# Kernel tuning notes

Hardware: AMD Instinct MI355X
Metric: run time of the kernel (lower is better)

The kernel has to match this reference:

```python
import jax, jax.numpy as jnp
import numpy as np

# Module constants (from init_kwargs / MoELayer branch for n_experts=8)
D_MODEL = 512
D_FF = 2048
N_HEADS = 8
N_EXPERTS = 8
TOP_K = 2
CAPACITY_FACTOR = 1.6  # n_experts > 6 branch
BATCH = 4096
SEQ = 16  # 4x4 board
LN_EPS = 1e-5


def setup_inputs() -> dict:
    key = jax.random.key(0)
    ks = jax.random.split(key, 24)
    s = 0.02
    d, f, e = D_MODEL, D_FF, N_EXPERTS
    inp = {
        'x': jax.random.normal(ks[0], (BATCH, SEQ, d), dtype=jnp.float32),
        'ln1_g': jnp.ones((d,), jnp.float32), 'ln1_b': jnp.zeros((d,), jnp.float32),
        'ln2_g': jnp.ones((d,), jnp.float32), 'ln2_b': jnp.zeros((d,), jnp.float32),
        # Linear weights stored [in, out] (equivalent to torch W.T)
        'wq': jax.random.normal(ks[1], (d, d)) * s, 'bq': jnp.zeros((d,)),
        'wk': jax.random.normal(ks[2], (d, d)) * s, 'bk': jnp.zeros((d,)),
        'wv': jax.random.normal(ks[3], (d, d)) * s, 'bv': jnp.zeros((d,)),
        'wo': jax.random.normal(ks[4], (d, d)) * s, 'bo': jnp.zeros((d,)),
        'router_w': jax.random.normal(ks[5], (d, e)) * s, 'router_b': jnp.zeros((e,)),
        'w1': jax.random.normal(ks[6], (e, d, f)) * s, 'b1': jnp.zeros((e, f)),
        'w2': jax.random.normal(ks[7], (e, f, d)) * s, 'b2': jnp.zeros((e, d)),
    }
    return inp


def _layernorm(x, g, b):
    mu = x.mean(-1, keepdims=True)
    var = ((x - mu) ** 2).mean(-1, keepdims=True)
    return (x - mu) * jax.lax.rsqrt(var + LN_EPS) * g + b


def _moe(xf, router_w, router_b, w1, b1, w2, b2):
    # xf: [T, D]
    T = xf.shape[0]
    probs = jax.nn.softmax(xf @ router_w + router_b, axis=-1)  # [T, E]
    _, topk_idx = jax.lax.top_k(probs, TOP_K)                  # [T, K]
    capacity = int(np.ceil(T * CAPACITY_FACTOR / N_EXPERTS))
    out = jnp.zeros_like(xf)
    tok = jnp.arange(T)
    for i in range(N_EXPERTS):
        mask = (topk_idx == i).any(-1)                 # token routed to expert i
        pos = jnp.where(mask, tok, T)                  # sentinel T for unrouted
        sel = jnp.sort(pos)[:capacity]                 # first `capacity` routed tokens, in token order
        xi = xf[jnp.minimum(sel, T - 1)]               # gather (padded rows unused)
        hi = jax.nn.gelu(xi @ w1[i] + b1[i], approximate=False)
        yi = hi @ w2[i] + b2[i]
        # scatter; OOB sentinel indices are dropped. Later experts overwrite
        # earlier ones for tokens routed to multiple experts (matches torch).
        out = out.at[sel].set(yi, mode='drop')
    return out


def reference(x, ln1_g, ln1_b, ln2_g, ln2_b, wq, bq, wk, bk, wv, bv, wo, bo,
              router_w, router_b, w1, b1, w2, b2):
    B, S, D = x.shape
    dk = D // N_HEADS
    # --- attention sublayer ---
    h = _layernorm(x, ln1_g, ln1_b)
    q = (h @ wq + bq).reshape(B, S, N_HEADS, dk)
    k = (h @ wk + bk).reshape(B, S, N_HEADS, dk)
    v = (h @ wv + bv).reshape(B, S, N_HEADS, dk)
    scores = jnp.einsum('bqhd,bkhd->bhqk', q, k) / np.sqrt(dk).astype(np.float32)
    attn = jax.nn.softmax(scores, axis=-1)
    ctx = jnp.einsum('bhqk,bkhd->bqhd', attn, v).reshape(B, S, D)
    x = x + ctx @ wo + bo
    # --- MoE sublayer ---
    h2 = _layernorm(x, ln2_g, ln2_b)
    moe_out = _moe(h2.reshape(-1, D), router_w, router_b, w1, b1, w2, b2)
    return x + moe_out.reshape(B, S, D)
```

## Files before the change

kernel.cpp:

```cpp
#include <hip/hip_runtime.h>
#include <hip/hip_bf16.h>
#include <math.h>

typedef unsigned short u16;
typedef unsigned int u32;
typedef _Float16 f16;
typedef __attribute__((ext_vector_type(8))) _Float16 f16x8;
typedef __attribute__((ext_vector_type(8))) short short8;
typedef __attribute__((ext_vector_type(4))) float f32x4;

#define TTOK 65536
#define QTOK 16384
#define CAP 13108
#define CAPP 13184

#define MFMA16(a, b, c) __builtin_amdgcn_mfma_f32_16x16x32_f16(a, b, c, 0, 0, 0)
#define MFMAB(a, b, c) __builtin_amdgcn_mfma_f32_16x16x32_bf16(a, b, c, 0, 0, 0)
#define LO_SCALE 2.44140625e-4f

#define SWZF(r) (((r) & 3) ^ ((((r) >> 2) & 1) << 1))

__device__ __forceinline__ u16 f2bf(float f) {
  union { float f; u32 u; } v; v.f = f;
  u32 r = v.u + 0x7fffu + ((v.u >> 16) & 1u);
  return (u16)(r >> 16);
}
__device__ __forceinline__ u16 f16b(f16 h) {
  union { f16 h; u16 u; } v; v.h = h; return v.u;
}
__device__ __forceinline__ f16 b2h(u16 u) {
  union { u16 s; f16 h; } v; v.s = u; return v.h;
}
__device__ __forceinline__ float gelu_f(float x) {
  float z = fabsf(x) * 0.70710678118654752f;
  float t = __builtin_amdgcn_rcpf(1.0f + 0.3275911f * z);
  float p = t * (0.254829592f + t * (-0.284496736f + t * (1.421413741f
          + t * (-1.453152027f + t * 1.061405429f))));
  float er = 1.0f - p * __expf(-z * z);
  er = (x < 0.0f) ? -er : er;
  return 0.5f * x * (1.0f + er);
}
__device__ __forceinline__ void gl16(const u16* g, u16* l) {
  __builtin_amdgcn_global_load_lds(
      (const __attribute__((address_space(1))) u32*)(const void*)g,
      (__attribute__((address_space(3))) u32*)(void*)l, 16, 0, 0);
}

__global__ __launch_bounds__(256) void prep1_kernel(
    const float* __restrict__ wq, const float* __restrict__ wk,
    const float* __restrict__ wv, const float* __restrict__ wo,
    const float* __restrict__ rw,
    u16* __restrict__ whi, u16* __restrict__ wlo, float* __restrict__ rwt)
{
  const int z = blockIdx.z;
  int idx = blockIdx.x * 256 + threadIdx.x;
  if (z == 4) {
    if (idx < 4096) {
      int n = idx >> 9, k = idx & 511;
      rwt[idx] = rw[k * 8 + n];
    }
    return;
  }
  const float* src = (z == 0) ? wq : (z == 1) ? wk : (z == 2) ? wv : wo;
  int n = idx >> 9, k = idx & 511;
  float v = src[k * 512 + n];
  f16 h = (f16)v;
  f16 l = (f16)((v - (float)h) * 4096.0f);
  whi[z * 262144 + idx] = f16b(h);
  wlo[z * 262144 + idx] = f16b(l);
}

__global__ __launch_bounds__(256) void prep2_kernel(
    const float* __restrict__ w1, const float* __restrict__ w2,
    u16* __restrict__ w1t, u16* __restrict__ w2t)
{
  __shared__ float tS[64][65];
  const int z = blockIdx.z;
  const float* src; u16* dst; int R, C;
  if (z < 8) { src = w1 + (size_t)z * 1048576; dst = w1t + (size_t)z * 1048576; R = 512; C = 2048; }
  else       { src = w2 + (size_t)(z - 8) * 1048576; dst = w2t + (size_t)(z - 8) * 1048576; R = 2048; C = 512; }
  const int tc = C >> 6;
  const int r0 = (blockIdx.x / tc) * 64, c0 = (blockIdx.x % tc) * 64;
  const int tid = threadIdx.x;
  #pragma unroll
  for (int j = 0; j < 16; ++j) {
    int idx = j * 256 + tid;
    int r = idx >> 6, c = idx & 63;
    tS[r][c] = src[(size_t)(r0 + r) * C + c0 + c];
  }
  __syncthreads();
  #pragma unroll
  for (int j = 0; j < 16; ++j) {
    int idx = j * 256 + tid;
    int c = idx >> 6, r = idx & 63;
    dst[(size_t)(c0 + c) * R + r0 + r] = f2bf(tS[r][c]);
  }
}

__global__ __launch_bounds__(256) void ln1_kernel(
    const float* __restrict__ x, const float* __restrict__ g,
    const float* __restrict__ b, u16* __restrict__ hh, u16* __restrict__ hl)
{
  const int row = blockIdx.x * 4 + (threadIdx.x >> 6);
  const int lane = threadIdx.x & 63;
  const float* xr = x + (size_t)row * 512 + lane * 8;
  float4 a = *(const float4*)xr;
  float4 c = *(const float4*)(xr + 4);
  double s1 = (double)a.x + a.y + a.z + a.w + c.x + c.y + c.z + c.w;
  double s2 = (double)a.x * a.x + (double)a.y * a.y + (double)a.z * a.z + (double)a.w * a.w
            + (double)c.x * c.x + (double)c.y * c.y + (double)c.z * c.z + (double)c.w * c.w;
  #pragma unroll
  for (int off = 32; off; off >>= 1) {
    s1 += __shfl_xor(s1, off, 64);
    s2 += __shfl_xor(s2, off, 64);
  }
  double mu = s1 * (1.0 / 512.0);
  double var = s2 * (1.0 / 512.0) - mu * mu;
  double rs = 1.0 / sqrt(var + 1e-5);
  float4 ga = *(const float4*)(g + lane * 8);
  float4 gb = *(const float4*)(g + lane * 8 + 4);
  float4 ba = *(const float4*)(b + lane * 8);
  float4 bb = *(const float4*)(b + lane * 8 + 4);
  float vv[8] = {a.x, a.y, a.z, a.w, c.x, c.y, c.z, c.w};
  float gg[8] = {ga.x, ga.y, ga.z, ga.w, gb.x, gb.y, gb.z, gb.w};
  float cc[8] = {ba.x, ba.y, ba.z, ba.w, bb.x, bb.y, bb.z, bb.w};
  u16 oh[8], ol[8];
  #pragma unroll
  for (int j = 0; j < 8; ++j) {
    float t = (float)(((double)vv[j] - mu) * rs);
    float n0 = t * gg[j] + cc[j];
    f16 h = (f16)n0;
    oh[j] = f16b(h);
    ol[j] = f16b((f16)((n0 - (float)h) * 4096.0f));
  }
  size_t base = (size_t)row * 512 + lane * 8;
  *(short8*)(hh + base) = *(const short8*)oh;
  *(short8*)(hl + base) = *(const short8*)ol;
}

__global__ __launch_bounds__(512, 2) void qkv_gemm_kernel(
    const u16* __restrict__ hh, const u16* __restrict__ hl,
    const u16* __restrict__ whi, const u16* __restrict__ wlo,
    const float* __restrict__ bq, const float* __restrict__ bk,
    const float* __restrict__ bv, u32* __restrict__ qkvh, int M0)
{
  __shared__ alignas(16) u16 SM[2][16384];
  const int tid = threadIdx.x;
  const int lane = tid & 63, w = tid >> 6;
  const int lid = blockIdx.x + 12 * blockIdx.y;
  const int c8 = lid & 7, kk = lid >> 3;
  const int rt = c8 * 16 + kk / 12;
  const int ct = kk % 12;
  const int col0 = ct * 128;
  const int row0 = rt * 128;
  const int wr = w >> 2, wc = w & 3;
  const int lr = lane & 15, lkq = lane >> 4;
  const int sx = (lkq ^ SWZF(lr)) * 8;
  const int lrow = lane >> 2;
  const int lcs = ((lane & 3) ^ SWZF(lrow)) * 8;

  const u16* gsrc[4];
  int loff[4];
  #pragma unroll
  for (int j = 0; j < 4; ++j) {
    const int q = w * 4 + j;
    loff[j] = q * 512;
    if (q < 8)       gsrc[j] = hh + (size_t)(M0 + row0 + q * 16 + lrow) * 512 + lcs;
    else if (q < 16) gsrc[j] = hl + (size_t)(M0 + row0 + (q - 8) * 16 + lrow) * 512 + lcs;
    else if (q < 24) gsrc[j] = whi + (size_t)(col0 + (q - 16) * 16 + lrow) * 512 + lcs;
    else             gsrc[j] = wlo + (size_t)(col0 + (q - 24) * 16 + lrow) * 512 + lcs;
  }

  f32x4 acch[4][2], accl[4][2];
  #pragma unroll
  for (int m = 0; m < 4; ++m)
    #pragma unroll
    for (int n = 0; n < 2; ++n) {
      f32x4 zz = {0.f, 0.f, 0.f, 0.f};
      acch[m][n] = zz; accl[m][n] = zz;
    }

  #pragma unroll
  for (int j = 0; j < 4; ++j) gl16(gsrc[j], &SM[0][loff[j]]);
  #pragma unroll
  for (int j = 0; j < 4; ++j) gl16(gsrc[j] + 32, &SM[1][loff[j]]);

  for (int kc = 0; kc < 16; ++kc) {
    if (kc == 15) asm volatile("s_waitcnt vmcnt(0)" ::: "memory");
    else          asm volatile("s_waitcnt vmcnt(4)" ::: "memory");
    __builtin_amdgcn_s_barrier();
    __builtin_amdgcn_sched_barrier(0);
    const u16* S = SM[kc & 1];
    f16x8 ah[4], al[4], bh[2], bl[2];
    #pragma unroll
    for (int m = 0; m < 4; ++m) {
      int r = wr * 64 + m * 16 + lr;
      ah[m] = *(const f16x8*)&S[r * 32 + sx];
      al[m] = *(const f16x8*)&S[4096 + r * 32 + sx];
    }
    #pragma unroll
    for (int n = 0; n < 2; ++n) {
      int c = wc * 32 + n * 16 + lr;
      bh[n] = *(const f16x8*)&S[8192 + c * 32 + sx];
      bl[n] = *(const f16x8*)&S[12288 + c * 32 + sx];
    }
    #pragma unroll
    for (int m = 0; m < 4; ++m)
      #pragma unroll
      for (int n = 0; n < 2; ++n) {
        acch[m][n] = MFMA16(ah[m], bh[n], acch[m][n]);
        accl[m][n] = MFMA16(ah[m], bl[n], accl[m][n]);
        accl[m][n] = MFMA16(al[m], bh[n], accl[m][n]);
      }
    __builtin_amdgcn_s_barrier();
    __builtin_amdgcn_sched_barrier(0);
    if (kc + 2 < 16) {
      #pragma unroll
      for (int j = 0; j < 4; ++j) gl16(gsrc[j] + (kc + 2) * 32, &SM[kc & 1][loff[j]]);
    }
  }
  #pragma unroll
  for (int m = 0; m < 4; ++m)
    #pragma unroll
    for (int n = 0; n < 2; ++n) {
      int col = col0 + wc * 32 + n * 16 + lr;
      float bb = (col < 512) ? bq[col] : (col < 1024) ? bk[col - 512] : bv[col - 1024];
      #pragma unroll
      for (int r = 0; r < 4; ++r) {
        int row = row0 + wr * 64 + m * 16 + lkq * 4 + r;
        float val = acch[m][n][r] + accl[m][n][r] * LO_SCALE + bb;
        f16 vh = (f16)val;
        f16 vl = (f16)((val - (float)vh) * 4096.0f);
        qkvh[(size_t)row * 1536 + col] = (u32)f16b(vh) | ((u32)f16b(vl) << 16);
      }
    }
}

__global__ __launch_bounds__(512) void attn_kernel(
    const u32* __restrict__ qkvh, u16* __restrict__ cth, u16* __restrict__ ctl)
{
  __shared__ alignas(16) u32 vS[16384];
  __shared__ float pS[8][16][17];

  const int tid = threadIdx.x;
  const int lane = tid & 63, w = tid >> 6;
  const int lr = lane & 15, lkq = lane >> 4;
  const int row0 = blockIdx.x * 32;

  #pragma unroll
  for (int i = 0; i < 8; ++i) {
    int chunk = w * 8 + i;
    const u32* src = qkvh + (size_t)(row0 + (chunk >> 1)) * 1536 + 1024 + (chunk & 1) * 256 + lane * 4;
    gl16((const u16*)src, (u16*)(vS + chunk * 256));
  }
  __syncthreads();

  const int h4 = w & 3, s = w >> 2;
  #pragma unroll
  for (int g = 0; g < 2; ++g) {
    const int h = g * 4 + h4;
    f16x8 qh[2], ql[2], kh[2], kl[2];
    #pragma unroll
    for (int dc = 0; dc < 2; ++dc) {
      const u32* qp = qkvh + (size_t)(row0 + s * 16 + lr) * 1536 + h * 64 + dc * 32 + lkq * 8;
      const u32* kp = qp + 512;
      uint4 q0 = *(const uint4*)qp, q1 = *(const uint4*)(qp + 4);
      uint4 k0 = *(const uint4*)kp, k1 = *(const uint4*)(kp + 4);
      u32 qu[8] = {q0.x, q0.y, q0.z, q0.w, q1.x, q1.y, q1.z, q1.w};
      u32 ku[8] = {k0.x, k0.y, k0.z, k0.w, k1.x, k1.y, k1.z, k1.w};
      #pragma unroll
      for (int i = 0; i < 8; ++i) {
        qh[dc][i] = b2h((u16)(qu[i] & 0xffffu)); ql[dc][i] = b2h((u16)(qu[i] >> 16));
        kh[dc][i] = b2h((u16)(ku[i] & 0xffffu)); kl[dc][i] = b2h((u16)(ku[i] >> 16));
      }
    }
    f32x4 sh = {0.f, 0.f, 0.f, 0.f}, sl = {0.f, 0.f, 0.f, 0.f};
    #pragma unroll
    for (int dc = 0; dc < 2; ++dc) {
      sh = MFMA16(qh[dc], kh[dc], sh);
      sl = MFMA16(qh[dc], kl[dc], sl);
      sl = MFMA16(ql[dc], kh[dc], sl);
    }
    float p_[4];
    #pragma unroll
    for (int r = 0; r < 4; ++r) {
      float sv = (sh[r] + sl[r] * LO_SCALE) * 0.125f;
      float mx = sv;
      #pragma unroll
      for (int off = 8; off; off >>= 1) mx = fmaxf(mx, __shfl_xor(mx, off, 16));
      float e = expf(sv - mx);
      float su = e;
      #pragma unroll
      for (int off = 8; off; off >>= 1) su += __shfl_xor(su, off, 16);
      p_[r] = e / su;
    }
    #pragma unroll
    for (int r = 0; r < 4; ++r) pS[w][lkq * 4 + r][lr] = p_[r];
    f16x8 pah, pal;
    #pragma unroll
    for (int jj = 0; jj < 8; ++jj) {
      float pv = (lkq < 2) ? pS[w][lr][lkq * 8 + jj] : 0.0f;
      f16 ph = (f16)pv;
      pah[jj] = ph;
      pal[jj] = (f16)((pv - (float)ph) * 4096.0f);
    }
    #pragma unroll
    for (int cf = 0; cf < 4; ++cf) {
      f16x8 vhf, vlf;
      #pragma unroll
      for (int jj = 0; jj < 8; ++jj) {
        u32 u = (lkq < 2) ? vS[(size_t)(s * 16 + lkq * 8 + jj) * 512 + h * 64 + cf * 16 + lr] : 0u;
        vhf[jj] = b2h((u16)(u & 0xffffu));
        vlf[jj] = b2h((u16)(u >> 16));
      }
      f32x4 ch = {0.f, 0.f, 0.f, 0.f}, cl = {0.f, 0.f, 0.f, 0.f};
      ch = MFMA16(pah, vhf, ch);
      cl = MFMA16(pah, vlf, cl);
      cl = MFMA16(pal, vhf, cl);
      #pragma unroll
      for (int r = 0; r < 4; ++r) {
        float cv = ch[r] + cl[r] * LO_SCALE;
        int row = row0 + s * 16 + lkq * 4 + r;
        int d = h * 64 + cf * 16 + lr;
        size_t gi = (size_t)row * 512 + d;
        f16 chv = (f16)cv;
        cth[gi] = f16b(chv);
        ctl[gi] = f16b((f16)((cv - (float)chv) * 4096.0f));
      }
    }
  }
}

__global__ __launch_bounds__(512, 2) void wo_gemm_kernel(
    const u16* __restrict__ cth, const u16* __restrict__ ctl,
    const u16* __restrict__ whi, const u16* __restrict__ wlo,
    const float* __restrict__ bo, const float* __restrict__ x,
    float* __restrict__ dout, int M0)
{
  __shared__ alignas(16) u16 SM[2][16384];
  const int tid = threadIdx.x;
  const int lane = tid & 63, w = tid >> 6;
  const int lid = blockIdx.x + 4 * blockIdx.y;
  const int c8 = lid & 7, kk = lid >> 3;
  const int rt = c8 * 16 + (kk >> 2), ct = kk & 3;
  const int col0 = ct * 128;
  const int row0 = rt * 128;
  const int wr = w >> 2, wc = w & 3;
  const int lr = lane & 15, lkq = lane >> 4;
  const int sx = (lkq ^ SWZF(lr)) * 8;
  const int lrow = lane >> 2;
  const int lcs = ((lane & 3) ^ SWZF(lrow)) * 8;

  const u16* wh3 = whi + 3 * 262144;
  const u16* wl3 = wlo + 3 * 262144;

  const u16* gsrc[4];
  int loff[4];
  #pragma unroll
  for (int j = 0; j < 4; ++j) {
    const int q = w * 4 + j;
    loff[j] = q * 512;
    if (q < 8)       gsrc[j] = cth + (size_t)(row0 + q * 16 + lrow) * 512 + lcs;
    else if (q < 16) gsrc[j] = ctl + (size_t)(row0 + (q - 8) * 16 + lrow) * 512 + lcs;
    else if (q < 24) gsrc[j] = wh3 + (size_t)(col0 + (q - 16) * 16 + lrow) * 512 + lcs;
    else             gsrc[j] = wl3 + (size_t)(col0 + (q - 24) * 16 + lrow) * 512 + lcs;
  }

  f32x4 acch[4][2], accl[4][2];
  #pragma unroll
  for (int m = 0; m < 4; ++m)
    #pragma unroll
    for (int n = 0; n < 2; ++n) {
      f32x4 zz = {0.f, 0.f, 0.f, 0.f};
      acch[m][n] = zz; accl[m][n] = zz;
    }

  #pragma unroll
  for (int j = 0; j < 4; ++j) gl16(gsrc[j], &SM[0][loff[j]]);
  #pragma unroll
  for (int j = 0; j < 4; ++j) gl16(gsrc[j] + 32, &SM[1][loff[j]]);

  for (int kc = 0; kc < 16; ++kc) {
    if (kc == 15) asm volatile("s_waitcnt vmcnt(0)" ::: "memory");
    else          asm volatile("s_waitcnt vmcnt(4)" ::: "memory");
    __builtin_amdgcn_s_barrier();
    __builtin_amdgcn_sched_barrier(0);
    const u16* S = SM[kc & 1];
    f16x8 ah[4], al[4], bh[2], bl[2];
    #pragma unroll
    for (int m = 0; m < 4; ++m) {
      int r = wr * 64 + m * 16 + lr;
      ah[m] = *(const f16x8*)&S[r * 32 + sx];
      al[m] = *(const f16x8*)&S[4096 + r * 32 + sx];
    }
    #pragma unroll
    for (int n = 0; n < 2; ++n) {
      int c = wc * 32 + n * 16 + lr;
      bh[n] = *(const f16x8*)&S[8192 + c * 32 + sx];
      bl[n] = *(const f16x8*)&S[12288 + c * 32 + sx];
    }
    #pragma unroll
    for (int m = 0; m < 4; ++m)
      #pragma unroll
      for (int n = 0; n < 2; ++n) {
        acch[m][n] = MFMA16(ah[m], bh[n], acch[m][n]);
        accl[m][n] = MFMA16(ah[m], bl[n], accl[m][n]);
        accl[m][n] = MFMA16(al[m], bh[n], accl[m][n]);
      }
    __builtin_amdgcn_s_barrier();
    __builtin_amdgcn_sched_barrier(0);
    if (kc + 2 < 16) {
      #pragma unroll
      for (int j = 0; j < 4; ++j) gl16(gsrc[j] + (kc + 2) * 32, &SM[kc & 1][loff[j]]);
    }
  }
  #pragma unroll
  for (int m = 0; m < 4; ++m)
    #pragma unroll
    for (int n = 0; n < 2; ++n) {
      int col = col0 + wc * 32 + n * 16 + lr;
      float bvv = bo[col];
      #pragma unroll
      for (int r = 0; r < 4; ++r) {
        int row = row0 + wr * 64 + m * 16 + lkq * 4 + r;
        float val = acch[m][n][r] + accl[m][n][r] * LO_SCALE + bvv;
        size_t gi = (size_t)(M0 + row) * 512 + col;
        dout[gi] = x[gi] + val;
      }
    }
}

__global__ __launch_bounds__(256) void router_kernel(
    const float* __restrict__ xp, const float* __restrict__ g2,
    const float* __restrict__ b2ln, const float* __restrict__ rwt,
    const float* __restrict__ rb, float* __restrict__ stats,
    int* __restrict__ t2, u16* __restrict__ xn)
{
  const int tid = threadIdx.x;
  const int lane = tid & 63, w = tid >> 6;
  const int tok = blockIdx.x * 4 + w;
  const float* xr = xp + (size_t)tok * 512 + lane * 8;
  float4 a = *(const float4*)(xr);
  float4 b = *(const float4*)(xr + 4);
  double s1 = (double)a.x + a.y + a.z + a.w + b.x + b.y + b.z + b.w;
  double s2 = (double)a.x * a.x + (double)a.y * a.y + (double)a.z * a.z + (double)a.w * a.w
            + (double)b.x * b.x + (double)b.y * b.y + (double)b.z * b.z + (double)b.w * b.w;
  #pragma unroll
  for (int off = 32; off; off >>= 1) {
    s1 += __shfl_xor(s1, off, 64);
    s2 += __shfl_xor(s2, off, 64);
  }
  double mu = s1 * (1.0 / 512.0);
  double var = s2 * (1.0 / 512.0) - mu * mu;
  double rs = 1.0 / sqrt(var + 1e-5);
  if (lane == 0) {
    stats[tok * 2] = (float)mu;
    stats[tok * 2 + 1] = (float)rs;
  }
  float4 ga = *(const float4*)(g2 + lane * 8);
  float4 gb = *(const float4*)(g2 + lane * 8 + 4);
  float4 ca = *(const float4*)(b2ln + lane * 8);
  float4 cb = *(const float4*)(b2ln + lane * 8 + 4);
  {
    float muf = (float)mu, rsf = (float)rs;
    u16 ox[8];
    ox[0] = f2bf((a.x - muf) * rsf * ga.x + ca.x);
    ox[1] = f2bf((a.y - muf) * rsf * ga.y + ca.y);
    ox[2] = f2bf((a.z - muf) * rsf * ga.z + ca.z);
    ox[3] = f2bf((a.w - muf) * rsf * ga.w + ca.w);
    ox[4] = f2bf((b.x - muf) * rsf * gb.x + cb.x);
    ox[5] = f2bf((b.y - muf) * rsf * gb.y + cb.y);
    ox[6] = f2bf((b.z - muf) * rsf * gb.z + cb.z);
    ox[7] = f2bf((b.w - muf) * rsf * gb.w + cb.w);
    *(short8*)(xn + (size_t)tok * 512 + lane * 8) = *(const short8*)ox;
  }
  float h[8];
  h[0] = (float)(((double)a.x - mu) * rs * (double)ga.x + (double)ca.x);
  h[1] = (float)(((double)a.y - mu) * rs * (double)ga.y + (double)ca.y);
  h[2] = (float)(((double)a.z - mu) * rs * (double)ga.z + (double)ca.z);
  h[3] = (float)(((double)a.w - mu) * rs * (double)ga.w + (double)ca.w);
  h[4] = (float)(((double)b.x - mu) * rs * (double)gb.x + (double)cb.x);
  h[5] = (float)(((double)b.y - mu) * rs * (double)gb.y + (double)cb.y);
  h[6] = (float)(((double)b.z - mu) * rs * (double)gb.z + (double)cb.z);
  h[7] = (float)(((double)b.w - mu) * rs * (double)gb.w + (double)cb.w);
  double acc[8];
  #pragma unroll
  for (int e = 0; e < 8; ++e) {
    const float* wp = rwt + e * 512 + lane * 8;
    float4 w0 = *(const float4*)wp;
    float4 w1 = *(const float4*)(wp + 4);
    acc[e] = (double)h[0] * (double)w0.x + (double)h[1] * (double)w0.y
           + (double)h[2] * (double)w0.z + (double)h[3] * (double)w0.w
           + (double)h[4] * (double)w1.x + (double)h[5] * (double)w1.y
           + (double)h[6] * (double)w1.z + (double)h[7] * (double)w1.w;
  }
  #pragma unroll
  for (int e = 0; e < 8; ++e) {
    acc[e] += __shfl_xor(acc[e], 8, 64);
    acc[e] += __shfl_xor(acc[e], 16, 64);
    acc[e] += __shfl_xor(acc[e], 32, 64);
  }
  const int b0 = lane & 1, b1 = (lane >> 1) & 1, b2_ = (lane >> 2) & 1;
  double t4[4];
  #pragma unroll
  for (int k = 0; k < 4; ++k) {
    double mine = b0 ? acc[2 * k + 1] : acc[2 * k];
    double send = b0 ? acc[2 * k] : acc[2 * k + 1];
    t4[k] = mine + __shfl_xor(send, 1, 64);
  }
  double u2[2];
  #pragma unroll
  for (int k = 0; k < 2; ++k) {
    double mine = b1 ? t4[2 * k + 1] : t4[2 * k];
    double send = b1 ? t4[2 * k] : t4[2 * k + 1];
    u2[k] = mine + __shfl_xor(send, 2, 64);
  }
  {
    double mine = b2_ ? u2[1] : u2[0];
    double send = b2_ ? u2[0] : u2[1];
    double tot = mine + __shfl_xor(send, 4, 64);
    const int e = lane & 7;
    double lg = tot + (double)rb[e];
    double vv = lg; int ix = e;
    #pragma unroll
    for (int off = 4; off; off >>= 1) {
      double ov = __shfl_xor(vv, off, 8);
      int oi = __shfl_xor(ix, off, 8);
      if (ov > vv || (ov == vv && oi < ix)) { vv = ov; ix = oi; }
    }
    double v2 = (e == ix) ? -1.0e300 : lg; int ix2 = e;
    #pragma unroll
    for (int off = 4; off; off >>= 1) {
      double ov = __shfl_xor(v2, off, 8);
      int oi = __shfl_xor(ix2, off, 8);
      if (ov > v2 || (ov == v2 && oi < ix2)) { v2 = ov; ix2 = oi; }
    }
    if (lane == 0) t2[tok] = ix | (ix2 << 8);
  }
}

__global__ __launch_bounds__(256) void scan1_kernel(
    const int* __restrict__ t2, int* __restrict__ blkcnt, int* __restrict__ ranks)
{
  __shared__ u32 mask[256];
  __shared__ u16 rk[256][8];
  const int t = threadIdx.x, tok = blockIdx.x * 256 + t;
  const int p = t2[tok];
  const int e1 = p & 0xff, e2 = (p >> 8) & 0xff;
  mask[t] = (1u << e1) | (1u << e2);
  __syncthreads();
  if (t < 8) {
    int c = 0;
    for (int i = 0; i < 256; ++i) { rk[i][t] = (u16)c; c += (mask[i] >> t) & 1u; }
    blkcnt[blockIdx.x * 8 + t] = c;
  }
  __syncthreads();
  ranks[tok] = (int)rk[t][e1] | ((int)rk[t][e2] << 16);
}

__global__ void scan2_kernel(const int* __restrict__ blkcnt,
                             int* __restrict__ offs, int* __restrict__ cnts)
{
  const int e = threadIdx.x;
  if (e < 8) {
    int off = 0;
    for (int b = 0; b < 256; ++b) { offs[b * 8 + e] = off; off += blkcnt[b * 8 + e]; }
    cnts[e] = off < CAP ? off : CAP;
  }
}

__global__ __launch_bounds__(256) void scan3_kernel(
    const int* __restrict__ t2, const int* __restrict__ ranks,
    const int* __restrict__ offs, int* __restrict__ list, int* __restrict__ win)
{
  const int t = threadIdx.x, blk = blockIdx.x, tok = blk * 256 + t;
  const int p = t2[tok];
  const int e1 = p & 0xff, e2 = (p >> 8) & 0xff;
  const int r = ranks[tok];
  const int r1 = r & 0xffff, r2 = (r >> 16) & 0xffff;
  const int s1 = offs[blk * 8 + e1] + r1;
  const int s2 = offs[blk * 8 + e2] + r2;
  int w = -1;
  if (s1 < CAP) { list[e1 * CAPP + s1] = tok; w = (e1 > w) ? e1 : w; }
  if (s2 < CAP) { list[e2 * CAPP + s2] = tok; w = (e2 > w) ? e2 : w; }
  win[tok] = w;
}

template<int EPI, int NKC, int AST, int BST, int NX>
__device__ __forceinline__ void ffn_body(
    int lid, u16* SMb,
    const u16* __restrict__ A, const u16* __restrict__ Bw,
    const float* __restrict__ bias, u16* __restrict__ outb,
    const int* __restrict__ list, const int* __restrict__ cnts,
    const int* __restrict__ win, float* __restrict__ dout, int ebase)
{
  const int c8 = lid & 7;
  const int kk = lid >> 3;
  const int wx = kk & (NX - 1);
  const int pr = kk / NX;
  const int wz = pr / 13;
  const int wy = c8 * 13 + pr % 13;
  if (wy >= 103) return;
  const int ez = wz;
  const int expert = ebase + ez;
  const int tid = threadIdx.x;
  const int lane = tid & 63, w = tid >> 6;
  const int colb = wx * 256;
  const int row0 = wy * 128;
  const int lr = lane & 15, lkq = lane >> 4;
  const int sx = (lkq ^ SWZF(lr)) * 8;
  const int lrow = lane >> 2;
  const int lcs = ((lane & 3) ^ SWZF(lrow)) * 8;

  const u16* Bp = Bw + (size_t)expert * 1048576;

  const u16* gsrc[6];
  int loff[6];
  #pragma unroll
  for (int j = 0; j < 2; ++j) {
    int q = w * 2 + j;
    int arow = row0 + q * 16 + lrow;
    if (EPI == 0) {
      int tok = list[(size_t)expert * CAPP + arow] & 65535;
      gsrc[j] = A + (size_t)tok * 512 + lcs;
    } else {
      gsrc[j] = A + (size_t)ez * CAPP * 2048 + (size_t)arow * AST + lcs;
    }
    loff[j] = q * 512;
  }
  #pragma unroll
  for (int j = 2; j < 6; ++j) {
    int q = w * 4 + (j - 2);
    gsrc[j] = Bp + (size_t)(colb + q * 16 + lrow) * BST + lcs;
    loff[j] = 4096 + q * 512;
  }

  f32x4 acc[8][4];
  #pragma unroll
  for (int m = 0; m < 8; ++m)
    #pragma unroll
    for (int n = 0; n < 4; ++n) {
      f32x4 zz = {0.f, 0.f, 0.f, 0.f};
      acc[m][n] = zz;
    }

  #pragma unroll
  for (int j = 0; j < 6; ++j) gl16(gsrc[j], &SMb[loff[j]]);
  #pragma unroll
  for (int j = 0; j < 6; ++j) gl16(gsrc[j] + 32, &SMb[12288 + loff[j]]);

  int cur = 0, nx2 = 2;
  for (int kc = 0; kc < NKC; ++kc) {
    if (kc == NKC - 1) asm volatile("s_waitcnt vmcnt(0)" ::: "memory");
    else               asm volatile("s_waitcnt vmcnt(6)" ::: "memory");
    __builtin_amdgcn_s_barrier();
    __builtin_amdgcn_sched_barrier(0);
    if (kc + 2 < NKC) {
      #pragma unroll
      for (int j = 0; j < 6; ++j) gl16(gsrc[j] + (kc + 2) * 32, &SMb[nx2 * 12288 + loff[j]]);
    }
    const u16* S = &SMb[cur * 12288];
    short8 af[8], bf[4];
    #pragma unroll
    for (int m = 0; m < 8; ++m)
      af[m] = *(const short8*)&S[(m * 16 + lr) * 32 + sx];
    #pragma unroll
    for (int n = 0; n < 4; ++n)
      bf[n] = *(const short8*)&S[4096 + (w * 64 + n * 16 + lr) * 32 + sx];
    #pragma unroll
    for (int m = 0; m < 8; ++m)
      #pragma unroll
      for (int n = 0; n < 4; ++n)
        acc[m][n] = MFMAB(af[m], bf[n], acc[m][n]);
    cur = (cur == 2) ? 0 : cur + 1;
    nx2 = (nx2 == 2) ? 0 : nx2 + 1;
  }

  if (EPI == 0) {
    #pragma unroll
    for (int m = 0; m < 8; ++m)
      #pragma unroll
      for (int n = 0; n < 4; ++n) {
        int col = colb + w * 64 + n * 16 + lr;
        float bvv = bias[expert * 2048 + col];
        #pragma unroll
        for (int r = 0; r < 4; ++r) {
          int row = row0 + m * 16 + lkq * 4 + r;
          float val = acc[m][n][r] + bvv;
          outb[(size_t)ez * CAPP * 2048 + (size_t)row * 2048 + col] = f2bf(gelu_f(val));
        }
      }
  } else {
    const int cnt = cnts[expert];
    const int* gidx = list + (size_t)expert * CAPP;
    #pragma unroll
    for (int m = 0; m < 8; ++m) {
      int rowb = row0 + m * 16 + lkq * 4;
      #pragma unroll
      for (int r = 0; r < 4; ++r) {
        int row = rowb + r;
        if (row < cnt) {
          int tok = gidx[row];
          if (win[tok] == expert) {
            #pragma unroll
            for (int n = 0; n < 4; ++n) {
              int col = colb + w * 64 + n * 16 + lr;
              float val = acc[m][n][r] + bias[expert * 512 + col];
              size_t oi = (size_t)tok * 512 + col;
              dout[oi] = dout[oi] + val;
            }
          }
        }
      }
    }
  }
}

__global__ __launch_bounds__(256, 2) void ffn_merged_kernel(
    const u16* __restrict__ xn, const u16* __restrict__ w1t,
    const float* __restrict__ b1, u16* __restrict__ hidW,
    const u16* __restrict__ hidR, const u16* __restrict__ w2t,
    const float* __restrict__ b2,
    const int* __restrict__ list, const int* __restrict__ cnts,
    const int* __restrict__ win, float* __restrict__ dout,
    int nb2, int eb1, int eb2)
{
  __shared__ alignas(16) u16 SM[3][12288];
  const int bx = blockIdx.x;
  if (bx < nb2) {
    ffn_body<1, 64, 2048, 2048, 2>(bx, &SM[0][0], hidR, w2t, b2, nullptr,
                                   list, cnts, win, dout, eb2);
  } else {
    ffn_body<0, 16, 512, 512, 8>(bx - nb2, &SM[0][0], xn, w1t, b1, hidW,
                                 list, cnts, nullptr, nullptr, eb1);
  }
}

extern "C" void kernel_launch(void* const* d_in, const int* in_sizes, int n_in,
                              void* d_out, int out_size, void* d_ws, size_t ws_size,
                              hipStream_t stream) {
  const float* x    = (const float*)d_in[0];
  const float* ln1g = (const float*)d_in[1];
  const float* ln1b = (const float*)d_in[2];
  const float* ln2g = (const float*)d_in[3];
  const float* ln2b = (const float*)d_in[4];
  const float* wq   = (const float*)d_in[5];
  const float* bq   = (const float*)d_in[6];
  const float* wk   = (const float*)d_in[7];
  const float* bk   = (const float*)d_in[8];
  const float* wv   = (const float*)d_in[9];
  const float* bv   = (const float*)d_in[10];
  const float* wo   = (const float*)d_in[11];
  const float* bo   = (const float*)d_in[12];
  const float* rw   = (const float*)d_in[13];
  const float* rb   = (const float*)d_in[14];
  const float* w1   = (const float*)d_in[15];
  const float* b1   = (const float*)d_in[16];
  const float* w2   = (const float*)d_in[17];
  const float* b2   = (const float*)d_in[18];
  float* dout = (float*)d_out;

  char* ws = (char*)d_ws;
  u16*   hh   = (u16*)(ws + 0LL);
  u16*   hl   = (u16*)(ws + 67108864LL);
  u32*   qkvh = (u32*)(ws + 134217728LL);
  u16*   cth  = (u16*)(ws + 234881024LL);
  u16*   ctl  = (u16*)(ws + 251658240LL);
  u16*   whi  = (u16*)(ws + 369098752LL);
  u16*   wlo  = (u16*)(ws + 371195904LL);
  float* rwt  = (float*)(ws + 373293056LL);
  float* st2  = (float*)(ws + 373309440LL);
  int*   t2   = (int*)(ws + 373833728LL);
  int*   rks  = (int*)(ws + 374095872LL);
  int*   bc   = (int*)(ws + 374358016LL);
  int*   offs = (int*)(ws + 374366208LL);
  int*   cnts = (int*)(ws + 374374400LL);
  int*   list = (int*)(ws + 374374464LL);
  int*   win  = (int*)(ws + 374796352LL);
  u16*   w1t  = (u16*)(ws + 0LL);
  u16*   w2t  = (u16*)(ws + 16777216LL);
  u16*   xn   = (u16*)(ws + 33554432LL);
  u16*   hid0 = (u16*)(ws + 100663296LL);
  u16*   hid1 = (u16*)(ws + 208666624LL);

  prep1_kernel<<<dim3(1024, 1, 5), 256, 0, stream>>>(wq, wk, wv, wo, rw, whi, wlo, rwt);
  ln1_kernel<<<16384, 256, 0, stream>>>(x, ln1g, ln1b, hh, hl);
  for (int q = 0; q < 4; ++q) {
    qkv_gemm_kernel<<<dim3(12, 128), 512, 0, stream>>>(
        hh, hl, whi, wlo, bq, bk, bv, qkvh, q * QTOK);
    attn_kernel<<<512, 512, 0, stream>>>(qkvh, cth, ctl);
    wo_gemm_kernel<<<dim3(4, 128), 512, 0, stream>>>(
        cth, ctl, whi, wlo, bo, x, dout, q * QTOK);
  }
  prep2_kernel<<<dim3(256, 1, 16), 256, 0, stream>>>(w1, w2, w1t, w2t);
  router_kernel<<<16384, 256, 0, stream>>>(dout, ln2g, ln2b, rwt, rb, st2, t2, xn);
  scan1_kernel<<<256, 256, 0, stream>>>(t2, bc, rks);
  scan2_kernel<<<1, 256, 0, stream>>>(bc, offs, cnts);
  scan3_kernel<<<256, 256, 0, stream>>>(t2, rks, offs, list, win);
  for (int s = 0; s < 5; ++s) {
    const int nb1 = (s < 4) ? 1664 : 0;
    const int nb2 = (s > 0) ? 416 : 0;
    u16* hw = (s & 1) ? hid1 : hid0;
    const u16* hr = ((s - 1) & 1) ? hid1 : hid0;
    ffn_merged_kernel<<<nb1 + nb2, 256, 0, stream>>>(
        xn, w1t, b1, hw, hr, w2t, b2, list, cnts, win, dout,
        nb2, s * 2, (s - 1) * 2);
  }
}
```

Measured before the change: 1.419 ms.

## Fuse wo GEMM of previous chunk with qkv GEMM of next chunk

The separate qkv and wo GEMM kernels become device functions that one combined kernel dispatches by block index. Each launch runs the wo projection for chunk q-1 together with the qkv projection for chunk q, with a prologue and an epilogue launch covering the ends. This cuts the number of kernel launches and fills the GPU better, since the small 512-block wo grid no longer runs alone. The risk is mixed workloads within one grid and a dependency on the ordering between attention and the qkvh/cth buffers.

```diff
diff --git a/kernel.cpp b/kernel.cpp
--- a/kernel.cpp
+++ b/kernel.cpp
@@ -138,16 +138,15 @@
   *(short8*)(hl + base) = *(const short8*)ol;
 }
 
-__global__ __launch_bounds__(512, 2) void qkv_gemm_kernel(
+__device__ __forceinline__ void qkv_body(
+    int lid, u16* SMb,
     const u16* __restrict__ hh, const u16* __restrict__ hl,
     const u16* __restrict__ whi, const u16* __restrict__ wlo,
     const float* __restrict__ bq, const float* __restrict__ bk,
     const float* __restrict__ bv, u32* __restrict__ qkvh, int M0)
 {
-  __shared__ alignas(16) u16 SM[2][16384];
   const int tid = threadIdx.x;
   const int lane = tid & 63, w = tid >> 6;
-  const int lid = blockIdx.x + 12 * blockIdx.y;
   const int c8 = lid & 7, kk = lid >> 3;
   const int rt = c8 * 16 + kk / 12;
   const int ct = kk % 12;
@@ -181,16 +180,16 @@
     }
 
   #pragma unroll
-  for (int j = 0; j < 4; ++j) gl16(gsrc[j], &SM[0][loff[j]]);
-  #pragma unroll
-  for (int j = 0; j < 4; ++j) gl16(gsrc[j] + 32, &SM[1][loff[j]]);
+  for (int j = 0; j < 4; ++j) gl16(gsrc[j], &SMb[loff[j]]);
+  #pragma unroll
+  for (int j = 0; j < 4; ++j) gl16(gsrc[j] + 32, &SMb[16384 + loff[j]]);
 
   for (int kc = 0; kc < 16; ++kc) {
     if (kc == 15) asm volatile("s_waitcnt vmcnt(0)" ::: "memory");
     else          asm volatile("s_waitcnt vmcnt(4)" ::: "memory");
     __builtin_amdgcn_s_barrier();
     __builtin_amdgcn_sched_barrier(0);
-    const u16* S = SM[kc & 1];
+    const u16* S = &SMb[(kc & 1) * 16384];
     f16x8 ah[4], al[4], bh[2], bl[2];
     #pragma unroll
     for (int m = 0; m < 4; ++m) {
@@ -216,7 +215,7 @@
     __builtin_amdgcn_sched_barrier(0);
     if (kc + 2 < 16) {
       #pragma unroll
-      for (int j = 0; j < 4; ++j) gl16(gsrc[j] + (kc + 2) * 32, &SM[kc & 1][loff[j]]);
+      for (int j = 0; j < 4; ++j) gl16(gsrc[j] + (kc + 2) * 32, &SMb[(kc & 1) * 16384 + loff[j]]);
     }
   }
   #pragma unroll
@@ -234,6 +233,122 @@
         qkvh[(size_t)row * 1536 + col] = (u32)f16b(vh) | ((u32)f16b(vl) << 16);
       }
     }
+}
+
+__device__ __forceinline__ void wo_body(
+    int lid, u16* SMb,
+    const u16* __restrict__ cth, const u16* __restrict__ ctl,
+    const u16* __restrict__ whi, const u16* __restrict__ wlo,
+    const float* __restrict__ bo, const float* __restrict__ x,
+    float* __restrict__ dout, int M0)
+{
+  const int tid = threadIdx.x;
+  const int lane = tid & 63, w = tid >> 6;
+  const int c8 = lid & 7, kk = lid >> 3;
+  const int rt = c8 * 16 + (kk >> 2), ct = kk & 3;
+  const int col0 = ct * 128;
+  const int row0 = rt * 128;
+  const int wr = w >> 2, wc = w & 3;
+  const int lr = lane & 15, lkq = lane >> 4;
+  const int sx = (lkq ^ SWZF(lr)) * 8;
+  const int lrow = lane >> 2;
+  const int lcs = ((lane & 3) ^ SWZF(lrow)) * 8;
+
+  const u16* wh3 = whi + 3 * 262144;
+  const u16* wl3 = wlo + 3 * 262144;
+
+  const u16* gsrc[4];
+  int loff[4];
+  #pragma unroll
+  for (int j = 0; j < 4; ++j) {
+    const int q = w * 4 + j;
+    loff[j] = q * 512;
+    if (q < 8)       gsrc[j] = cth + (size_t)(row0 + q * 16 + lrow) * 512 + lcs;
+    else if (q < 16) gsrc[j] = ctl + (size_t)(row0 + (q - 8) * 16 + lrow) * 512 + lcs;
+    else if (q < 24) gsrc[j] = wh3 + (size_t)(col0 + (q - 16) * 16 + lrow) * 512 + lcs;
+    else             gsrc[j] = wl3 + (size_t)(col0 + (q - 24) * 16 + lrow) * 512 + lcs;
+  }
+
+  f32x4 acch[4][2], accl[4][2];
+  #pragma unroll
+  for (int m = 0; m < 4; ++m)
+    #pragma unroll
+    for (int n = 0; n < 2; ++n) {
+      f32x4 zz = {0.f, 0.f, 0.f, 0.f};
+      acch[m][n] = zz; accl[m][n] = zz;
+    }
+
+  #pragma unroll
+  for (int j = 0; j < 4; ++j) gl16(gsrc[j], &SMb[loff[j]]);
+  #pragma unroll
+  for (int j = 0; j < 4; ++j) gl16(gsrc[j] + 32, &SMb[16384 + loff[j]]);
+
+  for (int kc = 0; kc < 16; ++kc) {
+    if (kc == 15) asm volatile("s_waitcnt vmcnt(0)" ::: "memory");
+    else          asm volatile("s_waitcnt vmcnt(4)" ::: "memory");
+    __builtin_amdgcn_s_barrier();
+    __builtin_amdgcn_sched_barrier(0);
+    const u16* S = &SMb[(kc & 1) * 16384];
+    f16x8 ah[4], al[4], bh[2], bl[2];
+    #pragma unroll
+    for (int m = 0; m < 4; ++m) {
+      int r = wr * 64 + m * 16 + lr;
+      ah[m] = *(const f16x8*)&S[r * 32 + sx];
+      al[m] = *(const f16x8*)&S[4096 + r * 32 + sx];
+    }
+    #pragma unroll
+    for (int n = 0; n < 2; ++n) {
+      int c = wc * 32 + n * 16 + lr;
+      bh[n] = *(const f16x8*)&S[8192 + c * 32 + sx];
+      bl[n] = *(const f16x8*)&S[12288 + c * 32 + sx];
+    }
+    #pragma unroll
+    for (int m = 0; m < 4; ++m)
+      #pragma unroll
+      for (int n = 0; n < 2; ++n) {
+        acch[m][n] = MFMA16(ah[m], bh[n], acch[m][n]);
+        accl[m][n] = MFMA16(ah[m], bl[n], accl[m][n]);
+        accl[m][n] = MFMA16(al[m], bh[n], accl[m][n]);
+      }
+    __builtin_amdgcn_s_barrier();
+    __builtin_amdgcn_sched_barrier(0);
+    if (kc + 2 < 16) {
+      #pragma unroll
+      for (int j = 0; j < 4; ++j) gl16(gsrc[j] + (kc + 2) * 32, &SMb[(kc & 1) * 16384 + loff[j]]);
+    }
+  }
+  #pragma unroll
+  for (int m = 0; m < 4; ++m)
+    #pragma unroll
+    for (int n = 0; n < 2; ++n) {
+      int col = col0 + wc * 32 + n * 16 + lr;
+      float bvv = bo[col];
+      #pragma unroll
+      for (int r = 0; r < 4; ++r) {
+        int row = row0 + wr * 64 + m * 16 + lkq * 4 + r;
+        float val = acch[m][n][r] + accl[m][n][r] * LO_SCALE + bvv;
+        size_t gi = (size_t)(M0 + row) * 512 + col;
+        dout[gi] = x[gi] + val;
+      }
+    }
+}
+
+__global__ __launch_bounds__(512, 2) void woqkv_kernel(
+    const u16* __restrict__ hh, const u16* __restrict__ hl,
+    const u16* __restrict__ cth, const u16* __restrict__ ctl,
+    const u16* __restrict__ whi, const u16* __restrict__ wlo,
+    const float* __restrict__ bq, const float* __restrict__ bk,
+    const float* __restrict__ bv, const float* __restrict__ bo,
+    const float* __restrict__ x, u32* __restrict__ qkvh,
+    float* __restrict__ dout, int nbW, int M0w, int M0q)
+{
+  __shared__ alignas(16) u16 SM[2][16384];
+  const int bx = blockIdx.x;
+  if (bx < nbW) {
+    wo_body(bx, &SM[0][0], cth, ctl, whi, wlo, bo, x, dout, M0w);
+  } else {
+    qkv_body(bx - nbW, &SM[0][0], hh, hl, whi, wlo, bq, bk, bv, qkvh, M0q);
+  }
 }
 
 __global__ __launch_bounds__(512) void attn_kernel(
@@ -329,105 +444,6 @@
       }
     }
   }
-}
-
-__global__ __launch_bounds__(512, 2) void wo_gemm_kernel(
-    const u16* __restrict__ cth, const u16* __restrict__ ctl,
-    const u16* __restrict__ whi, const u16* __restrict__ wlo,
-    const float* __restrict__ bo, const float* __restrict__ x,
-    float* __restrict__ dout, int M0)
-{
-  __shared__ alignas(16) u16 SM[2][16384];
-  const int tid = threadIdx.x;
-  const int lane = tid & 63, w = tid >> 6;
-  const int lid = blockIdx.x + 4 * blockIdx.y;
-  const int c8 = lid & 7, kk = lid >> 3;
-  const int rt = c8 * 16 + (kk >> 2), ct = kk & 3;
-  const int col0 = ct * 128;
-  const int row0 = rt * 128;
-  const int wr = w >> 2, wc = w & 3;
-  const int lr = lane & 15, lkq = lane >> 4;
-  const int sx = (lkq ^ SWZF(lr)) * 8;
-  const int lrow = lane >> 2;
-  const int lcs = ((lane & 3) ^ SWZF(lrow)) * 8;
-
-  const u16* wh3 = whi + 3 * 262144;
-  const u16* wl3 = wlo + 3 * 262144;
-
-  const u16* gsrc[4];
-  int loff[4];
-  #pragma unroll
-  for (int j = 0; j < 4; ++j) {
-    const int q = w * 4 + j;
-    loff[j] = q * 512;
-    if (q < 8)       gsrc[j] = cth + (size_t)(row0 + q * 16 + lrow) * 512 + lcs;
-    else if (q < 16) gsrc[j] = ctl + (size_t)(row0 + (q - 8) * 16 + lrow) * 512 + lcs;
-    else if (q < 24) gsrc[j] = wh3 + (size_t)(col0 + (q - 16) * 16 + lrow) * 512 + lcs;
-    else             gsrc[j] = wl3 + (size_t)(col0 + (q - 24) * 16 + lrow) * 512 + lcs;
-  }
-
-  f32x4 acch[4][2], accl[4][2];
-  #pragma unroll
-  for (int m = 0; m < 4; ++m)
-    #pragma unroll
-    for (int n = 0; n < 2; ++n) {
-      f32x4 zz = {0.f, 0.f, 0.f, 0.f};
-      acch[m][n] = zz; accl[m][n] = zz;
-    }
-
-  #pragma unroll
-  for (int j = 0; j < 4; ++j) gl16(gsrc[j], &SM[0][loff[j]]);
-  #pragma unroll
-  for (int j = 0; j < 4; ++j) gl16(gsrc[j] + 32, &SM[1][loff[j]]);
-
-  for (int kc = 0; kc < 16; ++kc) {
-    if (kc == 15) asm volatile("s_waitcnt vmcnt(0)" ::: "memory");
-    else          asm volatile("s_waitcnt vmcnt(4)" ::: "memory");
-    __builtin_amdgcn_s_barrier();
-    __builtin_amdgcn_sched_barrier(0);
-    const u16* S = SM[kc & 1];
-    f16x8 ah[4], al[4], bh[2], bl[2];
-    #pragma unroll
-    for (int m = 0; m < 4; ++m) {
-      int r = wr * 64 + m * 16 + lr;
-      ah[m] = *(const f16x8*)&S[r * 32 + sx];
-      al[m] = *(const f16x8*)&S[4096 + r * 32 + sx];
-    }
-    #pragma unroll
-    for (int n = 0; n < 2; ++n) {
-      int c = wc * 32 + n * 16 + lr;
-      bh[n] = *(const f16x8*)&S[8192 + c * 32 + sx];
-      bl[n] = *(const f16x8*)&S[12288 + c * 32 + sx];
-    }
-    #pragma unroll
-    for (int m = 0; m < 4; ++m)
-      #pragma unroll
-      for (int n = 0; n < 2; ++n) {
-        acch[m][n] = MFMA16(ah[m], bh[n], acch[m][n]);
-        accl[m][n] = MFMA16(ah[m], bl[n], accl[m][n]);
-        accl[m][n] = MFMA16(al[m], bh[n], accl[m][n]);
-      }
-    __builtin_amdgcn_s_barrier();
-    __builtin_amdgcn_sched_barrier(0);
-    if (kc + 2 < 16) {
-      #pragma unroll
-      for (int j = 0; j < 4; ++j) gl16(gsrc[j] + (kc + 2) * 32, &SM[kc & 1][loff[j]]);
-    }
-  }
-  #pragma unroll
-  for (int m = 0; m < 4; ++m)
-    #pragma unroll
-    for (int n = 0; n < 2; ++n) {
-      int col = col0 + wc * 32 + n * 16 + lr;
-      float bvv = bo[col];
-      #pragma unroll
-      for (int r = 0; r < 4; ++r) {
-        int row = row0 + wr * 64 + m * 16 + lkq * 4 + r;
-        float val = acch[m][n][r] + accl[m][n][r] * LO_SCALE + bvv;
-        size_t gi = (size_t)(M0 + row) * 512 + col;
-        dout[gi] = x[gi] + val;
-      }
-    }
 }
 
 __global__ __launch_bounds__(256) void router_kernel(
@@ -785,13 +801,18 @@
 
   prep1_kernel<<<dim3(1024, 1, 5), 256, 0, stream>>>(wq, wk, wv, wo, rw, whi, wlo, rwt);
   ln1_kernel<<<16384, 256, 0, stream>>>(x, ln1g, ln1b, hh, hl);
-  for (int q = 0; q < 4; ++q) {
-    qkv_gemm_kernel<<<dim3(12, 128), 512, 0, stream>>>(
-        hh, hl, whi, wlo, bq, bk, bv, qkvh, q * QTOK);
+  woqkv_kernel<<<1536, 512, 0, stream>>>(
+      hh, hl, cth, ctl, whi, wlo, bq, bk, bv, bo, x, qkvh, dout, 0, 0, 0);
+  attn_kernel<<<512, 512, 0, stream>>>(qkvh, cth, ctl);
+  for (int q = 1; q < 4; ++q) {
+    woqkv_kernel<<<2048, 512, 0, stream>>>(
+        hh, hl, cth, ctl, whi, wlo, bq, bk, bv, bo, x, qkvh, dout,
+        512, (q - 1) * QTOK, q * QTOK);
     attn_kernel<<<512, 512, 0, stream>>>(qkvh, cth, ctl);
-    wo_gemm_kernel<<<dim3(4, 128), 512, 0, stream>>>(
-        cth, ctl, whi, wlo, bo, x, dout, q * QTOK);
-  }
+  }
+  woqkv_kernel<<<512, 512, 0, stream>>>(
+      hh, hl, cth, ctl, whi, wlo, bq, bk, bv, bo, x, qkvh, dout,
+      512, 3 * QTOK, 0);
   prep2_kernel<<<dim3(256, 1, 16), 256, 0, stream>>>(w1, w2, w1t, w2t);
   router_kernel<<<16384, 256, 0, stream>>>(dout, ln2g, ln2b, rwt, rb, st2, t2, xn);
   scan1_kernel<<<256, 256, 0, stream>>>(t2, bc, rks);
```

Result: slower. 1.457 ms (+2.7%).
